# Performance work log

Measured on AMD Instinct MI355X. Metric: run time of the kernel, lower is better.

Reference implementation:

```python
import jax, jax.numpy as jnp
import numpy as np

B, S, D, H = 2, 2048, 1024, 16
DK = D // H


def setup_inputs() -> dict:
    key = jax.random.key(0)
    ks = jax.random.split(key, 8)
    scale = 1.0 / np.sqrt(D)
    inp = {
        "query": jax.random.normal(ks[0], (B, S, D), dtype=jnp.float32),
        "key": jax.random.normal(ks[1], (B, S, D), dtype=jnp.float32),
        "value": jax.random.normal(ks[2], (B, S, D), dtype=jnp.float32),
        # causal mask, broadcastable over batch and heads
        "mask": jnp.tril(jnp.ones((S, S), dtype=jnp.int32))[None, None, :, :],
        "W_q": jax.random.normal(ks[3], (D, D), dtype=jnp.float32) * scale,
        "W_k": jax.random.normal(ks[4], (D, D), dtype=jnp.float32) * scale,
        "W_v": jax.random.normal(ks[5], (D, D), dtype=jnp.float32) * scale,
        "W_o": jax.random.normal(ks[6], (D, D), dtype=jnp.float32) * scale,
    }
    return inp


def _split_heads(t):
    Bb, Ss, _ = t.shape
    return t.reshape(Bb, Ss, H, DK).transpose(0, 2, 1, 3)  # [B,H,S,DK]


def reference(query, key, value, mask, W_q, W_k, W_v, W_o):
    # Linear(d,d,bias=False): y = x @ W^T (torch stores weight as [out,in])
    Q = _split_heads(query @ W_q.T)
    K = _split_heads(key @ W_k.T)
    V = _split_heads(value @ W_v.T)
    scores = jnp.einsum("bhqd,bhkd->bhqk", Q, K) / jnp.sqrt(jnp.float32(DK))
    scores = jnp.where(mask == 0, -jnp.inf, scores)
    weights = jax.nn.softmax(scores, axis=-1)
    weights = jnp.nan_to_num(weights, nan=0.0)  # fully-masked rows -> 0
    # dropout is identity at inference
    x = jnp.einsum("bhqk,bhkd->bhqd", weights, V)
    x = x.transpose(0, 2, 1, 3).reshape(B, S, D)
    return x @ W_o.T
```

## Files before the change

### kernel.cpp

```cpp
#include <hip/hip_runtime.h>
#include <hip/hip_bf16.h>

#define D_MODEL 1024
#define NHEAD   16
#define HDK     64
#define SEQ     2048
#define BATCH   2
#define BS      (BATCH * SEQ)

typedef __attribute__((ext_vector_type(8))) short bf16x8;
typedef __attribute__((ext_vector_type(4))) float f32x4;
typedef __attribute__((ext_vector_type(4))) unsigned int u32x4;

__device__ __forceinline__ unsigned short f2bf(float f) {
    unsigned u = __builtin_bit_cast(unsigned, f);
    u += 0x7fffu + ((u >> 16) & 1u);
    return (unsigned short)(u >> 16);
}

__device__ __forceinline__ unsigned pack_hi(float x, float y) {
    return __builtin_amdgcn_perm(__builtin_bit_cast(unsigned, y),
                                 __builtin_bit_cast(unsigned, x), 0x07060302u);
}

__device__ __forceinline__ float exp2_fast(float x) {
    float r;
    asm("v_exp_f32 %0, %1" : "=v"(r) : "v"(x));
    return r;
}

typedef const void __attribute__((address_space(1))) gas_void;
typedef void __attribute__((address_space(3))) las_void;

__device__ __forceinline__ void gll16(const void* g, void* l) {
    __builtin_amdgcn_global_load_lds((gas_void*)g, (las_void*)l, 16, 0, 0);
}

__device__ __forceinline__ void cast_body(const float* __restrict__ src,
                                          unsigned short* __restrict__ dst, int i) {
    const float4* p = (const float4*)src + (size_t)i * 2;
    float4 a = p[0], b = p[1];
    ushort4 lo = make_ushort4(f2bf(a.x), f2bf(a.y), f2bf(a.z), f2bf(a.w));
    ushort4 hi = make_ushort4(f2bf(b.x), f2bf(b.y), f2bf(b.z), f2bf(b.w));
    ushort4* q = (ushort4*)dst + (size_t)i * 2;
    q[0] = lo; q[1] = hi;
}

__global__ __launch_bounds__(256)
void cast_act(const float* a, const float* b, const float* c,
              unsigned short* oa, unsigned short* ob, unsigned short* oc, int n8) {
    int i = blockIdx.x * 256 + threadIdx.x;
    if (i >= n8) return;
    const float* s = blockIdx.y == 0 ? a : blockIdx.y == 1 ? b : c;
    unsigned short* d = blockIdx.y == 0 ? oa : blockIdx.y == 1 ? ob : oc;
    cast_body(s, d, i);
}

__global__ __launch_bounds__(256)
void cast_wt(const float* a, const float* b, const float* c, const float* dd,
             unsigned short* oa, unsigned short* ob, unsigned short* oc, unsigned short* od, int n8) {
    int i = blockIdx.x * 256 + threadIdx.x;
    if (i >= n8) return;
    const float* s = blockIdx.y == 0 ? a : blockIdx.y == 1 ? b : blockIdx.y == 2 ? c : dd;
    unsigned short* d = blockIdx.y == 0 ? oa : blockIdx.y == 1 ? ob : blockIdx.y == 2 ? oc : od;
    cast_body(s, d, i);
}

__device__ __forceinline__ void gemm_kloop128(const unsigned short* __restrict__ X,
                                              const unsigned short* __restrict__ W,
                                              unsigned short* As, unsigned short* Bs,
                                              int bm, int bn, f32x4 acc[4][4]) {
    const int t    = threadIdx.x;
    const int w    = t >> 6;
    const int L    = t & 63;
    const int quad = L >> 4;
    const int lm   = L & 15;
    const int r8   = L >> 3;
    const int sl   = L & 7;
    const int xcol = ((sl ^ r8) & 7) * 8;
    const int wr   = (w >> 1) * 64;
    const int wc   = (w & 1) * 64;

    for (int kt = 0; kt < D_MODEL; kt += 64) {
        __syncthreads();
        #pragma unroll
        for (int i = 0; i < 4; ++i) {
            int c = w * 4 + i;
            gll16(X + (size_t)(bm + c * 8 + r8) * D_MODEL + kt + xcol, &As[c * 512]);
        }
        #pragma unroll
        for (int i = 0; i < 4; ++i) {
            int c = w * 4 + i;
            gll16(W + (size_t)(bn + c * 8 + r8) * D_MODEL + kt + xcol, &Bs[c * 512]);
        }
        __syncthreads();

        #pragma unroll
        for (int ch = 0; ch < 2; ++ch) {
            bf16x8 af[4], bfr[4];
            #pragma unroll
            for (int ms = 0; ms < 4; ++ms) {
                int row = wr + ms * 16 + lm;
                af[ms] = *(const bf16x8*)&As[row * 64 + (((ch * 4 + quad) ^ (row & 7)) * 8)];
            }
            #pragma unroll
            for (int ns = 0; ns < 4; ++ns) {
                int row = wc + ns * 16 + lm;
                bfr[ns] = *(const bf16x8*)&Bs[row * 64 + (((ch * 4 + quad) ^ (row & 7)) * 8)];
            }
            #pragma unroll
            for (int ms = 0; ms < 4; ++ms)
                #pragma unroll
                for (int ns = 0; ns < 4; ++ns)
                    acc[ms][ns] = __builtin_amdgcn_mfma_f32_16x16x32_bf16(
                        af[ms], bfr[ns], acc[ms][ns], 0, 0, 0);
        }
    }
}

__device__ __forceinline__ void gemm_kloop64(const unsigned short* __restrict__ X,
                                             const unsigned short* __restrict__ W,
                                             unsigned short* As, unsigned short* Bs,
                                             int bm, int bn, f32x4 acc[2][4]) {
    const int t    = threadIdx.x;
    const int w    = t >> 6;
    const int L    = t & 63;
    const int quad = L >> 4;
    const int lm   = L & 15;
    const int r8   = L >> 3;
    const int sl   = L & 7;
    const int xcol = ((sl ^ r8) & 7) * 8;

    for (int kt = 0; kt < D_MODEL; kt += 64) {
        __syncthreads();
        #pragma unroll
        for (int i = 0; i < 4; ++i) {
            int c = w * 4 + i;
            gll16(X + (size_t)(bm + c * 8 + r8) * D_MODEL + kt + xcol, &As[c * 512]);
        }
        #pragma unroll
        for (int i = 0; i < 2; ++i) {
            int c = w * 2 + i;
            gll16(W + (size_t)(bn + c * 8 + r8) * D_MODEL + kt + xcol, &Bs[c * 512]);
        }
        __syncthreads();

        #pragma unroll
        for (int ch = 0; ch < 2; ++ch) {
            bf16x8 af[2], bfr[4];
            #pragma unroll
            for (int ms = 0; ms < 2; ++ms) {
                int row = w * 32 + ms * 16 + lm;
                af[ms] = *(const bf16x8*)&As[row * 64 + (((ch * 4 + quad) ^ (row & 7)) * 8)];
            }
            #pragma unroll
            for (int ns = 0; ns < 4; ++ns) {
                int row = ns * 16 + lm;
                bfr[ns] = *(const bf16x8*)&Bs[row * 64 + (((ch * 4 + quad) ^ (row & 7)) * 8)];
            }
            #pragma unroll
            for (int ms = 0; ms < 2; ++ms)
                #pragma unroll
                for (int ns = 0; ns < 4; ++ns)
                    acc[ms][ns] = __builtin_amdgcn_mfma_f32_16x16x32_bf16(
                        af[ms], bfr[ns], acc[ms][ns], 0, 0, 0);
        }
    }
}

__global__ __launch_bounds__(256, 3)
void proj_gemm(const unsigned short* __restrict__ qx, const unsigned short* __restrict__ kx,
               const unsigned short* __restrict__ vx, const unsigned short* __restrict__ wq,
               const unsigned short* __restrict__ wk, const unsigned short* __restrict__ wv,
               unsigned short* __restrict__ Qp, unsigned short* __restrict__ Kp,
               unsigned short* __restrict__ VT) {
    __shared__ __align__(16) unsigned short As[128 * 64];
    __shared__ __align__(16) unsigned short Bs[128 * 64];

    const int p = blockIdx.z;
    const unsigned short* X = p == 0 ? qx : p == 1 ? kx : vx;
    const unsigned short* W = p == 0 ? wq : p == 1 ? wk : wv;
    const int bm = blockIdx.y * 128, bn = blockIdx.x * 128;

    f32x4 acc[4][4];
    #pragma unroll
    for (int ms = 0; ms < 4; ++ms)
        #pragma unroll
        for (int ns = 0; ns < 4; ++ns)
            acc[ms][ns] = (f32x4){0.f, 0.f, 0.f, 0.f};

    gemm_kloop128(X, W, As, Bs, bm, bn, acc);

    const int t = threadIdx.x, w = t >> 6, L = t & 63, quad = L >> 4, lm = L & 15;
    const int wr = (w >> 1) * 64, wc = (w & 1) * 64;
    if (p == 2) {
        const int b    = bm >> 11;
        const int s_in = (bm & (SEQ - 1)) + wr;
        #pragma unroll
        for (int ms = 0; ms < 4; ++ms)
            #pragma unroll
            for (int ns = 0; ns < 4; ++ns) {
                int dg = bn + wc + ns * 16 + lm;
                int h  = dg >> 6, d = dg & 63;
                ushort4 pk = make_ushort4(f2bf(acc[ms][ns][0]), f2bf(acc[ms][ns][1]),
                                          f2bf(acc[ms][ns][2]), f2bf(acc[ms][ns][3]));
                *(ushort4*)&VT[((size_t)((b * NHEAD + h) * HDK + d)) * SEQ +
                               s_in + ms * 16 + quad * 4] = pk;
            }
    } else {
        unsigned short* Y = p == 0 ? Qp : Kp;
        const float scl = p == 0 ? 0.18033688011112042f : 1.0f;
        #pragma unroll
        for (int ms = 0; ms < 4; ++ms)
            #pragma unroll
            for (int ns = 0; ns < 4; ++ns)
                #pragma unroll
                for (int r = 0; r < 4; ++r)
                    Y[(size_t)(bm + wr + ms * 16 + quad * 4 + r) * D_MODEL +
                      bn + wc + ns * 16 + lm] = f2bf(acc[ms][ns][r] * scl);
    }
}

__global__ __launch_bounds__(256)
void out_gemm(const unsigned short* __restrict__ X, const unsigned short* __restrict__ W,
              float* __restrict__ Y) {
    __shared__ __align__(16) unsigned short As[128 * 64];
    __shared__ __align__(16) unsigned short Bs[64 * 64];
    const int bm = blockIdx.y * 128, bn = blockIdx.x * 64;

    f32x4 acc[2][4];
    #pragma unroll
    for (int ms = 0; ms < 2; ++ms)
        #pragma unroll
        for (int ns = 0; ns < 4; ++ns)
            acc[ms][ns] = (f32x4){0.f, 0.f, 0.f, 0.f};

    gemm_kloop64(X, W, As, Bs, bm, bn, acc);

    const int t = threadIdx.x, w = t >> 6, L = t & 63, quad = L >> 4, lm = L & 15;
    #pragma unroll
    for (int ms = 0; ms < 2; ++ms)
        #pragma unroll
        for (int ns = 0; ns < 4; ++ns)
            #pragma unroll
            for (int r = 0; r < 4; ++r)
                Y[(size_t)(bm + w * 32 + ms * 16 + quad * 4 + r) * D_MODEL +
                  bn + ns * 16 + lm] = acc[ms][ns][r];
}

__global__ __launch_bounds__(256, 4)
void attn_mfma(const unsigned short* __restrict__ Q, const unsigned short* __restrict__ K,
               const unsigned short* __restrict__ VT, unsigned short* __restrict__ A) {
    __shared__ __align__(16) unsigned short Ks[2][64 * 64];
    __shared__ __align__(16) unsigned short Vs[2][64 * 64];

    const int t    = threadIdx.x;
    const int w    = t >> 6;
    const int L    = t & 63;
    const int quad = L >> 4;
    const int lm   = L & 15;
    const int r8   = L >> 3;
    const int sl   = L & 7;
    const int xcol = (sl ^ r8) * 8;

    const int id  = blockIdx.x;
    const int u   = id & 255;
    const int p   = id >> 8;
    const int qb_ = u >> 3;
    const int qt  = p == 0 ? qb_
                  : p == 1 ? 31 - qb_
                  : p == 2 ? (qb_ + 16) & 31
                           : (15 - qb_) & 31;
    const int bh  = (u & 7) | (p << 3);
    const int h   = bh & 15;
    const int b   = bh >> 4;

    const size_t hb   = (size_t)b * SEQ * D_MODEL + h * HDK;
    const size_t vrow = (size_t)(b * NHEAD + h) * HDK * SEQ;

    const unsigned short* kbase = K + hb;
    const unsigned short* vbase = VT + vrow;

    const int q0   = qt * 64;
    const int qrow = q0 + w * 16 + lm;

    auto stage = [&](int k0, int buf) {
        #pragma unroll
        for (int i = 0; i < 2; ++i) {
            int row = (w * 2 + i) * 8 + r8;
            gll16(kbase + (size_t)(k0 + row) * D_MODEL + xcol, &Ks[buf][(w * 2 + i) * 512]);
            gll16(vbase + (size_t)row * SEQ + k0 + xcol,       &Vs[buf][(w * 2 + i) * 512]);
        }
    };

    stage(0, 0);

    bf16x8 Qf0, Qf1;
    {
        const unsigned short* qp = Q + hb + (size_t)qrow * D_MODEL + quad * 8;
        Qf0 = *(const bf16x8*)qp;
        Qf1 = *(const bf16x8*)(qp + 32);
    }

    f32x4 Oacc[4];
    #pragma unroll
    for (int nt = 0; nt < 4; ++nt) Oacc[nt] = (f32x4){0.f, 0.f, 0.f, 0.f};
    float m_run  = -INFINITY;
    float l_lane = 0.f;

    __syncthreads();

    int bb = 0;
    for (int kt = 0; kt <= qt; ++kt) {
        const int k0 = kt * 64;
        const unsigned short* Kc = Ks[bb];
        const unsigned short* Vc = Vs[bb];
        if (kt < qt) stage(k0 + 64, bb ^ 1);

        f32x4 S[4];
        __builtin_amdgcn_s_setprio(1);
        #pragma unroll
        for (int ct = 0; ct < 4; ++ct) {
            bf16x8 a0 = *(const bf16x8*)&Kc[(ct * 16 + lm) * 64 + ((quad ^ (lm & 7)) * 8)];
            bf16x8 a1 = *(const bf16x8*)&Kc[(ct * 16 + lm) * 64 + (((4 + quad) ^ (lm & 7)) * 8)];
            f32x4 z = (f32x4){0.f, 0.f, 0.f, 0.f};
            z = __builtin_amdgcn_mfma_f32_16x16x32_bf16(a0, Qf0, z, 0, 0, 0);
            z = __builtin_amdgcn_mfma_f32_16x16x32_bf16(a1, Qf1, z, 0, 0, 0);
            S[ct] = z;
        }
        __builtin_amdgcn_s_setprio(0);

        if (k0 + 63 > q0 + w * 16) {
            #pragma unroll
            for (int ct = 0; ct < 4; ++ct)
                #pragma unroll
                for (int r = 0; r < 4; ++r)
                    if ((k0 + ct * 16 + quad * 4 + r) > qrow)
                        S[ct][r] = -1e30f;
        }

        float ml = fmaxf(fmaxf(fmaxf(S[0][0], S[0][1]), fmaxf(S[0][2], S[0][3])),
                         fmaxf(fmaxf(S[1][0], S[1][1]), fmaxf(S[1][2], S[1][3])));
        ml = fmaxf(ml, fmaxf(fmaxf(fmaxf(S[2][0], S[2][1]), fmaxf(S[2][2], S[2][3])),
                             fmaxf(fmaxf(S[3][0], S[3][1]), fmaxf(S[3][2], S[3][3]))));
        if (__any(ml > m_run + 8.0f)) {
            float m = fmaxf(ml, __shfl_xor(ml, 16));
            m = fmaxf(m, __shfl_xor(m, 32));
            const float m_new = fmaxf(m_run, m);
            const float alpha = exp2_fast(m_run - m_new);
            #pragma unroll
            for (int nt = 0; nt < 4; ++nt)
                #pragma unroll
                for (int r = 0; r < 4; ++r) Oacc[nt][r] *= alpha;
            l_lane *= alpha;
            m_run = m_new;
        }
        float psum = 0.f;
        #pragma unroll
        for (int ct = 0; ct < 4; ++ct)
            #pragma unroll
            for (int r = 0; r < 4; ++r) {
                float e = exp2_fast(S[ct][r] - m_run);
                S[ct][r] = e;
                psum += e;
            }
        l_lane += psum;

        unsigned x0 = pack_hi(S[0][0], S[0][1]);
        unsigned x1 = pack_hi(S[0][2], S[0][3]);
        unsigned y0 = pack_hi(S[1][0], S[1][1]);
        unsigned y1 = pack_hi(S[1][2], S[1][3]);
        asm("v_permlane32_swap_b32 %0, %1" : "+v"(x0), "+v"(y0));
        asm("v_permlane32_swap_b32 %0, %1" : "+v"(x1), "+v"(y1));
        asm("v_permlane16_swap_b32 %0, %1" : "+v"(x0), "+v"(y0));
        asm("v_permlane16_swap_b32 %0, %1" : "+v"(x1), "+v"(y1));
        bf16x8 Pb0 = __builtin_bit_cast(bf16x8, (u32x4){x0, x1, y0, y1});
        unsigned x2 = pack_hi(S[2][0], S[2][1]);
        unsigned x3 = pack_hi(S[2][2], S[2][3]);
        unsigned y2 = pack_hi(S[3][0], S[3][1]);
        unsigned y3 = pack_hi(S[3][2], S[3][3]);
        asm("v_permlane32_swap_b32 %0, %1" : "+v"(x2), "+v"(y2));
        asm("v_permlane32_swap_b32 %0, %1" : "+v"(x3), "+v"(y3));
        asm("v_permlane16_swap_b32 %0, %1" : "+v"(x2), "+v"(y2));
        asm("v_permlane16_swap_b32 %0, %1" : "+v"(x3), "+v"(y3));
        bf16x8 Pb1 = __builtin_bit_cast(bf16x8, (u32x4){x2, x3, y2, y3});

        __builtin_amdgcn_s_setprio(1);
        #pragma unroll
        for (int nt = 0; nt < 4; ++nt) {
            bf16x8 a0 = *(const bf16x8*)&Vc[(nt * 16 + lm) * 64 + ((quad ^ (lm & 7)) * 8)];
            bf16x8 a1 = *(const bf16x8*)&Vc[(nt * 16 + lm) * 64 + (((4 + quad) ^ (lm & 7)) * 8)];
            f32x4 o = Oacc[nt];
            o = __builtin_amdgcn_mfma_f32_16x16x32_bf16(a0, Pb0, o, 0, 0, 0);
            o = __builtin_amdgcn_mfma_f32_16x16x32_bf16(a1, Pb1, o, 0, 0, 0);
            Oacc[nt] = o;
        }
        __builtin_amdgcn_s_setprio(0);

        __syncthreads();
        bb ^= 1;
    }

    float l = l_lane + __shfl_xor(l_lane, 16);
    l += __shfl_xor(l, 32);
    const float inv_l = 1.f / l;
    unsigned short* es = &Ks[0][w * 1024];
    #pragma unroll
    for (int nt = 0; nt < 4; ++nt) {
        ushort4 pk = make_ushort4(f2bf(Oacc[nt][0] * inv_l), f2bf(Oacc[nt][1] * inv_l),
                                  f2bf(Oacc[nt][2] * inv_l), f2bf(Oacc[nt][3] * inv_l));
        int lc = 2 * nt + (quad >> 1);
        *(ushort4*)&es[lm * 64 + ((lc ^ (lm & 7)) * 8) + (quad & 1) * 4] = pk;
    }
    #pragma unroll
    for (int pp = 0; pp < 2; ++pp) {
        int qr = pp * 8 + r8;
        int dc = sl * 8;
        uint4 val = *(const uint4*)&es[qr * 64 + ((sl ^ (qr & 7)) * 8)];
        *(uint4*)&A[hb + (size_t)(q0 + w * 16 + qr) * D_MODEL + dc] = val;
    }
}

extern "C" void kernel_launch(void* const* d_in, const int* in_sizes, int n_in,
                              void* d_out, int out_size, void* d_ws, size_t ws_size,
                              hipStream_t stream) {
    const float* q  = (const float*)d_in[0];
    const float* k  = (const float*)d_in[1];
    const float* v  = (const float*)d_in[2];
    const float* Wq = (const float*)d_in[4];
    const float* Wk = (const float*)d_in[5];
    const float* Wv = (const float*)d_in[6];
    const float* Wo = (const float*)d_in[7];
    float* out = (float*)d_out;

    char* ws = (char*)d_ws;
    const size_t MB = 1024 * 1024;
    unsigned short* qb  = (unsigned short*)(ws + 0 * MB);
    unsigned short* kb  = (unsigned short*)(ws + 8 * MB);
    unsigned short* vb  = (unsigned short*)(ws + 16 * MB);
    unsigned short* wqb = (unsigned short*)(ws + 24 * MB);
    unsigned short* wkb = (unsigned short*)(ws + 26 * MB);
    unsigned short* wvb = (unsigned short*)(ws + 28 * MB);
    unsigned short* wob = (unsigned short*)(ws + 30 * MB);
    unsigned short* Qp  = (unsigned short*)(ws + 32 * MB);
    unsigned short* Kp  = (unsigned short*)(ws + 40 * MB);
    unsigned short* VTp = (unsigned short*)(ws + 48 * MB);
    unsigned short* Ap  = (unsigned short*)(ws + 56 * MB);

    const int nX8 = BS * D_MODEL / 8;
    const int nW8 = D_MODEL * D_MODEL / 8;
    cast_act<<<dim3(nX8 / 256, 3), 256, 0, stream>>>(q, k, v, qb, kb, vb, nX8);
    cast_wt <<<dim3(nW8 / 256, 4), 256, 0, stream>>>(Wq, Wk, Wv, Wo, wqb, wkb, wvb, wob, nW8);

    proj_gemm<<<dim3(D_MODEL / 128, BS / 128, 3), 256, 0, stream>>>(
        qb, kb, vb, wqb, wkb, wvb, Qp, Kp, VTp);

    attn_mfma<<<dim3(1024), 256, 0, stream>>>(Qp, Kp, VTp, Ap);

    out_gemm<<<dim3(D_MODEL / 64, BS / 128), 256, 0, stream>>>(Ap, wob, out);
}
```

Before: 218.8 us.

## Split long causal query tiles across two blocks and merge partial results

Query tiles 16-31 are split along the key dimension into two blocks, each writing unnormalized fp32 partial outputs plus row max and sum to workspace. A new combine kernel rescales and merges the two partials into bf16 attention output. Short tiles run whole, scheduled longest-first. This targets the load imbalance of causal attention at the cost of an extra launch and fp32 partial traffic. It also reorganizes the max and sum reductions into max3 and tree form.

```diff
diff --git a/kernel.cpp b/kernel.cpp
--- a/kernel.cpp
+++ b/kernel.cpp
@@ -27,6 +27,10 @@
     float r;
     asm("v_exp_f32 %0, %1" : "=v"(r) : "v"(x));
     return r;
+}
+
+__device__ __forceinline__ float max3(float a, float b, float c) {
+    return fmaxf(fmaxf(a, b), c);
 }
 
 typedef const void __attribute__((address_space(1))) gas_void;
@@ -250,7 +254,8 @@
 
 __global__ __launch_bounds__(256, 4)
 void attn_mfma(const unsigned short* __restrict__ Q, const unsigned short* __restrict__ K,
-               const unsigned short* __restrict__ VT, unsigned short* __restrict__ A) {
+               const unsigned short* __restrict__ VT, unsigned short* __restrict__ A,
+               float* __restrict__ PO, float* __restrict__ PML) {
     __shared__ __align__(16) unsigned short Ks[2][64 * 64];
     __shared__ __align__(16) unsigned short Vs[2][64 * 64];
 
@@ -263,17 +268,26 @@
     const int sl   = L & 7;
     const int xcol = (sl ^ r8) * 8;
 
-    const int id  = blockIdx.x;
-    const int u   = id & 255;
-    const int p   = id >> 8;
-    const int qb_ = u >> 3;
-    const int qt  = p == 0 ? qb_
-                  : p == 1 ? 31 - qb_
-                  : p == 2 ? (qb_ + 16) & 31
-                           : (15 - qb_) & 31;
-    const int bh  = (u & 7) | (p << 3);
-    const int h   = bh & 15;
-    const int b   = bh >> 4;
+    const int id = blockIdx.x;
+    int qt, bh, k_lo, k_hi, slot;
+    if (id < 1024) {
+        qt = 31 - (id >> 6);
+        const int j    = id & 63;
+        const int half = j >> 5;
+        bh = j & 31;
+        const int c = (qt + 2) >> 1;
+        k_lo = half ? c : 0;
+        k_hi = half ? qt + 1 : c;
+        slot = ((qt - 16) * 32 + bh) * 2 + half;
+    } else {
+        const int j = id - 1024;
+        qt = 15 - (j >> 5);
+        bh = j & 31;
+        k_lo = 0; k_hi = qt + 1;
+        slot = -1;
+    }
+    const int h = bh & 15;
+    const int b = bh >> 4;
 
     const size_t hb   = (size_t)b * SEQ * D_MODEL + h * HDK;
     const size_t vrow = (size_t)(b * NHEAD + h) * HDK * SEQ;
@@ -293,7 +307,7 @@
         }
     };
 
-    stage(0, 0);
+    stage(k_lo * 64, 0);
 
     bf16x8 Qf0, Qf1;
     {
@@ -311,11 +325,11 @@
     __syncthreads();
 
     int bb = 0;
-    for (int kt = 0; kt <= qt; ++kt) {
+    for (int kt = k_lo; kt < k_hi; ++kt) {
         const int k0 = kt * 64;
         const unsigned short* Kc = Ks[bb];
         const unsigned short* Vc = Vs[bb];
-        if (kt < qt) stage(k0 + 64, bb ^ 1);
+        if (kt + 1 < k_hi) stage((kt + 1) * 64, bb ^ 1);
 
         f32x4 S[4];
         __builtin_amdgcn_s_setprio(1);
@@ -339,10 +353,13 @@
                         S[ct][r] = -1e30f;
         }
 
-        float ml = fmaxf(fmaxf(fmaxf(S[0][0], S[0][1]), fmaxf(S[0][2], S[0][3])),
-                         fmaxf(fmaxf(S[1][0], S[1][1]), fmaxf(S[1][2], S[1][3])));
-        ml = fmaxf(ml, fmaxf(fmaxf(fmaxf(S[2][0], S[2][1]), fmaxf(S[2][2], S[2][3])),
-                             fmaxf(fmaxf(S[3][0], S[3][1]), fmaxf(S[3][2], S[3][3]))));
+        float ma = max3(S[0][0], S[0][1], S[0][2]);
+        float mb = max3(S[0][3], S[1][0], S[1][1]);
+        float mc = max3(S[1][2], S[1][3], S[2][0]);
+        float md = max3(S[2][1], S[2][2], S[2][3]);
+        float me = max3(S[3][0], S[3][1], S[3][2]);
+        float ml = max3(max3(ma, mb, mc), md, me);
+        ml = fmaxf(ml, S[3][3]);
         if (__any(ml > m_run + 8.0f)) {
             float m = fmaxf(ml, __shfl_xor(ml, 16));
             m = fmaxf(m, __shfl_xor(m, 32));
@@ -355,16 +372,18 @@
             l_lane *= alpha;
             m_run = m_new;
         }
-        float psum = 0.f;
         #pragma unroll
         for (int ct = 0; ct < 4; ++ct)
             #pragma unroll
-            for (int r = 0; r < 4; ++r) {
-                float e = exp2_fast(S[ct][r] - m_run);
-                S[ct][r] = e;
-                psum += e;
-            }
-        l_lane += psum;
+            for (int r = 0; r < 4; ++r)
+                S[ct][r] = exp2_fast(S[ct][r] - m_run);
+        {
+            float p0 = (S[0][0] + S[0][1]) + (S[0][2] + S[0][3]);
+            float p1 = (S[1][0] + S[1][1]) + (S[1][2] + S[1][3]);
+            float p2 = (S[2][0] + S[2][1]) + (S[2][2] + S[2][3]);
+            float p3 = (S[3][0] + S[3][1]) + (S[3][2] + S[3][3]);
+            l_lane += (p0 + p1) + (p2 + p3);
+        }
 
         unsigned x0 = pack_hi(S[0][0], S[0][1]);
         unsigned x1 = pack_hi(S[0][2], S[0][3]);
@@ -401,14 +420,83 @@
         bb ^= 1;
     }
 
-    float l = l_lane + __shfl_xor(l_lane, 16);
-    l += __shfl_xor(l, 32);
-    const float inv_l = 1.f / l;
-    unsigned short* es = &Ks[0][w * 1024];
+    float l_row = l_lane + __shfl_xor(l_lane, 16);
+    l_row += __shfl_xor(l_row, 32);
+
+    if (slot >= 0) {
+        float4* po = (float4*)(PO + (size_t)slot * 4096);
+        #pragma unroll
+        for (int nt = 0; nt < 4; ++nt)
+            po[t * 4 + nt] = __builtin_bit_cast(float4, Oacc[nt]);
+        if (quad == 0) {
+            PML[slot * 128 + w * 16 + lm]      = m_run;
+            PML[slot * 128 + 64 + w * 16 + lm] = l_row;
+        }
+    } else {
+        const float inv_l = 1.f / l_row;
+        unsigned short* es = &Ks[0][w * 1024];
+        #pragma unroll
+        for (int nt = 0; nt < 4; ++nt) {
+            ushort4 pk = make_ushort4(f2bf(Oacc[nt][0] * inv_l), f2bf(Oacc[nt][1] * inv_l),
+                                      f2bf(Oacc[nt][2] * inv_l), f2bf(Oacc[nt][3] * inv_l));
+            int lc = 2 * nt + (quad >> 1);
+            *(ushort4*)&es[lm * 64 + ((lc ^ (lm & 7)) * 8) + (quad & 1) * 4] = pk;
+        }
+        #pragma unroll
+        for (int pp = 0; pp < 2; ++pp) {
+            int qr = pp * 8 + r8;
+            int dc = sl * 8;
+            uint4 val = *(const uint4*)&es[qr * 64 + ((sl ^ (qr & 7)) * 8)];
+            *(uint4*)&A[hb + (size_t)(q0 + w * 16 + qr) * D_MODEL + dc] = val;
+        }
+    }
+}
+
+__global__ __launch_bounds__(256)
+void attn_combine(const float* __restrict__ PO, const float* __restrict__ PML,
+                  unsigned short* __restrict__ A) {
+    __shared__ __align__(16) unsigned short es_[4][16 * 64];
+
+    const int t    = threadIdx.x;
+    const int w    = t >> 6;
+    const int L    = t & 63;
+    const int quad = L >> 4;
+    const int lm   = L & 15;
+    const int r8   = L >> 3;
+    const int sl   = L & 7;
+
+    const int r  = blockIdx.x;
+    const int qt = 16 + (r >> 5);
+    const int bh = r & 31;
+    const int h  = bh & 15;
+    const int b  = bh >> 4;
+    const size_t hb = (size_t)b * SEQ * D_MODEL + h * HDK;
+    const int q0 = qt * 64;
+    const int q  = w * 16 + lm;
+
+    const float* ml1 = PML + (size_t)(r * 2 + 0) * 128;
+    const float* ml2 = PML + (size_t)(r * 2 + 1) * 128;
+    const float m1 = ml1[q], l1 = ml1[64 + q];
+    const float m2 = ml2[q], l2 = ml2[64 + q];
+    const float M  = fmaxf(m1, m2);
+    const float e1 = exp2_fast(m1 - M);
+    const float e2 = exp2_fast(m2 - M);
+    const float inv = 1.f / (e1 * l1 + e2 * l2);
+    const float c1 = e1 * inv, c2 = e2 * inv;
+
+    const float4* o1 = (const float4*)(PO + (size_t)(r * 2 + 0) * 4096);
+    const float4* o2 = (const float4*)(PO + (size_t)(r * 2 + 1) * 4096);
+
+    unsigned short* es = &es_[w][0];
     #pragma unroll
     for (int nt = 0; nt < 4; ++nt) {
-        ushort4 pk = make_ushort4(f2bf(Oacc[nt][0] * inv_l), f2bf(Oacc[nt][1] * inv_l),
-                                  f2bf(Oacc[nt][2] * inv_l), f2bf(Oacc[nt][3] * inv_l));
+        float4 a = o1[t * 4 + nt];
+        float4 c = o2[t * 4 + nt];
+        float v0 = a.x * c1 + c.x * c2;
+        float v1 = a.y * c1 + c.y * c2;
+        float v2 = a.z * c1 + c.z * c2;
+        float v3 = a.w * c1 + c.w * c2;
+        ushort4 pk = make_ushort4(f2bf(v0), f2bf(v1), f2bf(v2), f2bf(v3));
         int lc = 2 * nt + (quad >> 1);
         *(ushort4*)&es[lm * 64 + ((lc ^ (lm & 7)) * 8) + (quad & 1) * 4] = pk;
     }
@@ -446,6 +534,8 @@
     unsigned short* Kp  = (unsigned short*)(ws + 40 * MB);
     unsigned short* VTp = (unsigned short*)(ws + 48 * MB);
     unsigned short* Ap  = (unsigned short*)(ws + 56 * MB);
+    float* PO  = (float*)(ws + 0 * MB);
+    float* PML = (float*)(ws + 16 * MB);
 
     const int nX8 = BS * D_MODEL / 8;
     const int nW8 = D_MODEL * D_MODEL / 8;
@@ -455,7 +545,8 @@
     proj_gemm<<<dim3(D_MODEL / 128, BS / 128, 3), 256, 0, stream>>>(
         qb, kb, vb, wqb, wkb, wvb, Qp, Kp, VTp);
 
-    attn_mfma<<<dim3(1024), 256, 0, stream>>>(Qp, Kp, VTp, Ap);
+    attn_mfma<<<dim3(1536), 256, 0, stream>>>(Qp, Kp, VTp, Ap, PO, PML);
+    attn_combine<<<dim3(512), 256, 0, stream>>>(PO, PML, Ap);
 
     out_gemm<<<dim3(D_MODEL / 64, BS / 128), 256, 0, stream>>>(Ap, wob, out);
 }
```

After: 216.9 us. About the same (-0.9%).
